# Optimization experiments

Measured on AMD Instinct MI355X. Metric: run time of the kernel, lower is better.

The kernel has to match this reference:

```python
import jax, jax.numpy as jnp
import numpy as np

N_E = 1024
E_DIM = 256
BETA = 0.25


def setup_inputs() -> dict:
    key = jax.random.key(0)
    k1, k2 = jax.random.split(key)
    z = jax.random.normal(k1, (16, E_DIM, 64, 64), dtype=jnp.float32)
    # nn.Embedding weight init: uniform(-1/n_e, 1/n_e)
    embedding = jax.random.uniform(
        k2, (N_E, E_DIM), dtype=jnp.float32, minval=-1.0 / N_E, maxval=1.0 / N_E
    )
    return {"z": z, "embedding": embedding}


def reference(z, embedding):
    n_e, e_dim = embedding.shape
    # 'b c ... -> b ... c'
    zt = jnp.moveaxis(z, 1, -1)  # [B, H, W, C]
    zf = zt.reshape(-1, e_dim)   # [N, C]
    # squared distances ||zf||^2 + ||e||^2 - 2 zf e^T  -> [N, n_e]
    d = (
        jnp.sum(zf * zf, axis=1, keepdims=True)
        + jnp.sum(embedding * embedding, axis=1)
        - 2.0 * (zf @ embedding.T)
    )
    idx = jnp.argmin(d, axis=1)  # [N] int32
    # direct embedding gather (equivalent to one-hot @ embedding)
    z_q = embedding[idx].reshape(zt.shape)  # [B, H, W, C]
    # commitment / codebook loss (reduction='mean')
    loss = jnp.mean((jax.lax.stop_gradient(z_q) - zt) ** 2) + BETA * jnp.mean(
        (z_q - jax.lax.stop_gradient(zt)) ** 2
    )
    # straight-through estimator
    z_q_st = zt + jax.lax.stop_gradient(z_q - zt)
    # perplexity from code usage histogram (equals mean of one-hot rows)
    counts = jnp.zeros((n_e,), dtype=jnp.float32).at[idx].add(1.0)
    e_mean = counts / zf.shape[0]
    perplexity = jnp.exp(-jnp.sum(e_mean * jnp.log(e_mean + 1e-10)))
    # 'b ... c -> b c ...'
    z_q_out = jnp.moveaxis(z_q_st, -1, 1)  # [B, C, H, W]
    return z_q_out, loss, perplexity, idx
```

## Files before the change

kernel.cpp:

```cpp
#include <hip/hip_runtime.h>

typedef _Float16 half8 __attribute__((ext_vector_type(8)));
typedef float f32x16 __attribute__((ext_vector_type(16)));

#define EDIM 256
#define NE   1024
#define HW   4096

#define ZQ_OFF   0
#define LOSS_OFF 16777216
#define PERP_OFF 16777217
#define IDX_OFF  16777218

#define WS_ESPH    0
#define WS_BNORM   (1024*1024)
#define WS_COUNTS  (WS_BNORM + 4096)
#define WS_COUNTER (WS_COUNTS + 4096)
#define WS_LOSS    (WS_COUNTER + 16)
#define WS_AN      (WS_LOSS + 16)
#define WS_IDX     (WS_AN + 65536*4)
#define WS_LIST    (WS_IDX + 65536*4)
#define WS_ET      (WS_LIST + 65536*4)

#define EPS 3.0e-4f
#define GEPS (512.0f * EPS)

__device__ __forceinline__ float np_half128(const float* __restrict__ p, long stride) {
#pragma clang fp contract(off)
    float r[8];
#pragma unroll
    for (int j = 0; j < 8; ++j) { float v = p[(long)j * stride]; r[j] = v * v; }
    for (int i = 8; i < 128; i += 8) {
#pragma unroll
        for (int j = 0; j < 8; ++j) { float v = p[(long)(i + j) * stride]; r[j] += v * v; }
    }
    return ((r[0] + r[1]) + (r[2] + r[3])) + ((r[4] + r[5]) + (r[6] + r[7]));
}

__global__ void k_prep_e(const float* __restrict__ e, _Float16* __restrict__ eh) {
    int t = blockIdx.x * 256 + threadIdx.x;
    int j = t >> 8, c = t & 255;
    float v = e[t] * 1024.0f;
    _Float16 h = (_Float16)v;
    int jt = j >> 7, nt = (j >> 5) & 3, lm = j & 31;
    int kc = c >> 5, r = c & 31, kh = r >> 4, hb = (r >> 3) & 1, kk = r & 7;
    int chunk = (((jt * 8 + kc) * 4 + nt) * 2 + kh) * 64 + hb * 32 + lm;
    eh[chunk * 8 + kk] = h;
}

__global__ void k_transpose(const float* __restrict__ e, float* __restrict__ eT) {
    __shared__ float tile[32][257];
    int b = blockIdx.x;
    int t = threadIdx.x;
#pragma unroll
    for (int i = 0; i < 32; ++i)
        tile[i][t] = e[(size_t)(32 * b + i) * 256 + t];
    __syncthreads();
    int jl = t & 31, cg = t >> 5;
#pragma unroll
    for (int k = 0; k < 32; ++k) {
        int c = cg * 32 + k;
        eT[(size_t)c * 1024 + 32 * b + jl] = tile[jl][c];
    }
}

__global__ void k_bnorm(const float* __restrict__ e, float* __restrict__ Bn) {
    int j = blockIdx.x * 256 + threadIdx.x;
    const float* p = e + (size_t)j * EDIM;
    Bn[j] = np_half128(p, 1) + np_half128(p + 128, 1);
}

__global__ void k_rownorm(const float* __restrict__ z, float* __restrict__ An,
                          double* __restrict__ loss_sum) {
    __shared__ double ls[4];
    int t = threadIdx.x;
    int n = blockIdx.x * 256 + t;
    int b = n >> 12, hw = n & 4095;
    const float* p = z + (size_t)b * (EDIM * HW) + hw;
    float a = np_half128(p, HW) + np_half128(p + (size_t)128 * HW, HW);
    An[n] = a;
    double s = (double)a;
#pragma unroll
    for (int sh = 1; sh < 64; sh <<= 1) s += __shfl_xor(s, sh, 64);
    if ((t & 63) == 0) ls[t >> 6] = s;
    __syncthreads();
    if (t == 0) atomicAdd(loss_sum, (ls[0] + ls[1]) + (ls[2] + ls[3]));
}

__global__ __launch_bounds__(512, 2) void k_dist(
    const float* __restrict__ z, const _Float16* __restrict__ eh,
    const float* __restrict__ Bn, int* __restrict__ idxw,
    float* __restrict__ out, int* __restrict__ counter, int* __restrict__ list,
    double* __restrict__ loss_sum, int* __restrict__ counts)
{
    __shared__ uint4  sB[2][4096];
    __shared__ double lsum[16];
    __shared__ int    lflag[256];
    __shared__ int    lcnt;
    __shared__ int    lbase;

    const int t  = threadIdx.x;
    const int w  = t >> 6;
    const int L  = t & 63;
    const int l5 = L & 31;
    const int hb = L >> 5;
    const int n0 = blockIdx.x * 256;
    const int b  = n0 >> 12, hw0 = n0 & 4095;
    const float* zb = z + (size_t)b * (EDIM * HW) + hw0;
    const int rbase = w * 32;

    if (t == 0) lcnt = 0;

    const uint4* gB4 = (const uint4*)eh;
    const int wb = t & 448;

#pragma unroll
    for (int i = 0; i < 8; ++i)
        __builtin_amdgcn_global_load_lds(
            (const __attribute__((address_space(1))) void*)(gB4 + (0 * 4096 + i * 512 + t)),
            (__attribute__((address_space(3))) void*)(&sB[0][i * 512 + wb]),
            16, 0, 0);

    half8 Ah[16];
    {
        int m = rbase + l5;
#pragma unroll
        for (int ks = 0; ks < 16; ++ks) {
            float av[8];
#pragma unroll
            for (int j = 0; j < 8; ++j)
                av[j] = zb[(ks * 16 + hb * 8 + j) * HW + m];
#pragma unroll
            for (int j = 0; j < 8; ++j)
                Ah[ks][j] = (_Float16)av[j];
        }
    }

    f32x16 acc[4];
#pragma unroll
    for (int nt = 0; nt < 4; ++nt)
#pragma unroll
        for (int r = 0; r < 16; ++r) acc[nt][r] = 0.f;

    float g1[16], g2[16]; int i1[16];
#pragma unroll
    for (int r = 0; r < 16; ++r) { g1[r] = -1e30f; g2[r] = -1e30f; i1[r] = 0; }

    __syncthreads();

    for (int jt = 0; jt < 8; ++jt) {
        const int buf = jt & 1;
        if (jt < 7) {
#pragma unroll
            for (int i = 0; i < 8; ++i)
                __builtin_amdgcn_global_load_lds(
                    (const __attribute__((address_space(1))) void*)(gB4 + ((jt + 1) * 4096 + i * 512 + t)),
                    (__attribute__((address_space(3))) void*)(&sB[buf ^ 1][i * 512 + wb]),
                    16, 0, 0);
        }

#pragma unroll
        for (int kc = 0; kc < 8; ++kc) {
#pragma unroll
            for (int kh = 0; kh < 2; ++kh) {
#pragma unroll
                for (int nt = 0; nt < 4; ++nt) {
                    half8 bh = *(const half8*)&sB[buf][((kc * 4 + nt) * 2 + kh) * 64 + L];
                    acc[nt] = __builtin_amdgcn_mfma_f32_32x32x16_f16(
                        Ah[kc * 2 + kh], bh, acc[nt], 0, 0, 0);
                }
            }
        }

        float en512[4];
#pragma unroll
        for (int nt = 0; nt < 4; ++nt)
            en512[nt] = 512.0f * Bn[jt * 128 + nt * 32 + l5];
#pragma unroll
        for (int nt = 0; nt < 4; ++nt) {
            int jc = jt * 128 + nt * 32 + l5;
#pragma unroll
            for (int r = 0; r < 16; ++r) {
                float v = acc[nt][r] - en512[nt];
                g2[r] = fmaxf(g2[r], fminf(v, g1[r]));
                bool gt = v > g1[r];
                g1[r] = fmaxf(v, g1[r]);
                i1[r] = gt ? jc : i1[r];
                acc[nt][r] = 0.f;
            }
        }

        __syncthreads();
    }

    double lossP = 0.0;
#pragma unroll
    for (int r = 0; r < 16; ++r) {
        float v1 = g1[r], v2 = g2[r]; int ii = i1[r];
#pragma unroll
        for (int s = 1; s < 32; s <<= 1) {
            float o1 = __shfl_xor(v1, s, 64);
            int   oi = __shfl_xor(ii, s, 64);
            float o2 = __shfl_xor(v2, s, 64);
            float lo = fminf(v1, o1);
            if (o1 > v1 || (o1 == v1 && oi < ii)) { v1 = o1; ii = oi; }
            v2 = fmaxf(fmaxf(v2, o2), lo);
        }
        if (l5 == 0) {
            int rloc = rbase + 4 * hb + (r & 3) + 8 * (r >> 2);
            int n = n0 + rloc;
            idxw[n] = ii;
            out[IDX_OFF + n] = (float)ii;
            atomicAdd(&counts[ii], 1);
            lossP += -(double)v1 * (1.0 / 512.0);
            if (v1 - v2 < GEPS) {
                int p = atomicAdd(&lcnt, 1);
                if (p < 256) lflag[p] = n;
            }
        }
    }
    if (l5 == 0) lsum[w * 2 + hb] = lossP;
    __syncthreads();
    if (t == 0) {
        double s = 0.0;
#pragma unroll
        for (int i = 0; i < 16; ++i) s += lsum[i];
        atomicAdd(loss_sum, s);
        lbase = lcnt ? atomicAdd(counter, lcnt) : 0;
    }
    __syncthreads();
    for (int i = t; i < lcnt; i += 512) {
        int p = lbase + i;
        if (p < 65536) list[p] = lflag[i];
    }
}

__global__ __launch_bounds__(256, 2) void k_refine(
    const float* __restrict__ z, const float* __restrict__ eT,
    const float* __restrict__ Bn, const float* __restrict__ An,
    const int* __restrict__ counter, const int* __restrict__ list,
    int* __restrict__ idxw, float* __restrict__ out,
    int* __restrict__ counts)
{
    __shared__ float zs[8][256];
    __shared__ int   ns[8];
    __shared__ float ans[8];
    __shared__ float pv[4][8];
    __shared__ int   pi[4][8];
    int t = threadIdx.x;
    int cnt = min(*counter, 65536);
    for (int li0 = blockIdx.x * 8; li0 < cnt; li0 += gridDim.x * 8) {
        int nrows = min(8, cnt - li0);
        __syncthreads();
        if (t < 8) {
            int n = (t < nrows) ? list[li0 + t] : list[li0];
            ns[t] = n; ans[t] = An[n];
        }
        __syncthreads();
#pragma unroll
        for (int u = 0; u < 8; ++u) {
            int n = ns[u];
            zs[u][t] = z[(size_t)(n >> 12) * (EDIM * HW) + (n & 4095) + t * HW];
        }
        __syncthreads();

        float D[4][8];
#pragma unroll
        for (int q = 0; q < 4; ++q)
#pragma unroll
            for (int r = 0; r < 8; ++r) D[q][r] = 0.f;

        for (int c4 = 0; c4 < 64; ++c4) {
            float4 ec[4];
#pragma unroll
            for (int cc = 0; cc < 4; ++cc)
                ec[cc] = *(const float4*)&eT[(size_t)(c4 * 4 + cc) * 1024 + 4 * t];
            float4 zr[8];
#pragma unroll
            for (int r = 0; r < 8; ++r)
                zr[r] = *(const float4*)&zs[r][c4 * 4];
#pragma unroll
            for (int cc = 0; cc < 4; ++cc) {
                const float* ep = (const float*)&ec[cc];
#pragma unroll
                for (int r = 0; r < 8; ++r) {
                    float zv = ((const float*)&zr[r])[cc];
                    D[0][r] = __builtin_fmaf(ep[0], zv, D[0][r]);
                    D[1][r] = __builtin_fmaf(ep[1], zv, D[1][r]);
                    D[2][r] = __builtin_fmaf(ep[2], zv, D[2][r]);
                    D[3][r] = __builtin_fmaf(ep[3], zv, D[3][r]);
                }
            }
        }

        float bm[8]; int bi[8];
#pragma unroll
        for (int r = 0; r < 8; ++r) { bm[r] = 1e30f; bi[r] = 1 << 30; }
        float4 bn4 = *(const float4*)&Bn[4 * t];
        {
#pragma clang fp contract(off)
#pragma unroll
            for (int q = 0; q < 4; ++q) {
                float bnj = ((const float*)&bn4)[q];
                int j = 4 * t + q;
#pragma unroll
                for (int r = 0; r < 8; ++r) {
                    float t2 = D[q][r] + D[q][r];
                    float s  = ans[r] + bnj;
                    float d  = s - t2;
                    if (d < bm[r]) { bm[r] = d; bi[r] = j; }
                }
            }
        }
        int wv = t >> 6, L = t & 63;
#pragma unroll
        for (int r = 0; r < 8; ++r) {
            float v = bm[r]; int ii = bi[r];
#pragma unroll
            for (int s = 1; s < 64; s <<= 1) {
                float ov = __shfl_xor(v, s, 64);
                int   oi = __shfl_xor(ii, s, 64);
                if (ov < v || (ov == v && oi < ii)) { v = ov; ii = oi; }
            }
            if (L == 0) { pv[wv][r] = v; pi[wv][r] = ii; }
        }
        __syncthreads();
        if (t < nrows) {
            float v = pv[0][t]; int ii = pi[0][t];
#pragma unroll
            for (int w2 = 1; w2 < 4; ++w2)
                if (pv[w2][t] < v || (pv[w2][t] == v && pi[w2][t] < ii)) { v = pv[w2][t]; ii = pi[w2][t]; }
            int n = ns[t];
            int old = idxw[n];
            if (old != ii) {
                idxw[n] = ii;
                out[IDX_OFF + n] = (float)ii;
                atomicSub(&counts[old], 1);
                atomicAdd(&counts[ii], 1);
            }
        }
    }
}

__global__ void k_gather(const float* __restrict__ e, const int* __restrict__ idxw,
                         float* __restrict__ out) {
    __shared__ int   jrow[256];
    __shared__ float Ls[8][260];
    int t = threadIdx.x;
    int rg = blockIdx.x >> 1, ch = blockIdx.x & 1;
    int n0 = rg * 256;
    int b = n0 >> 12, hw0 = n0 & 4095;
    jrow[t] = idxw[n0 + t];
    float* zqb = out + ZQ_OFF + (size_t)b * (EDIM * HW) + hw0 + (size_t)ch * 128 * HW;
    int w = t >> 6, L = t & 63;
    __syncthreads();

    for (int cc = 0; cc < 16; ++cc) {
        const float4* ep = (const float4*)(e + (size_t)jrow[t] * EDIM + ch * 128 + cc * 8);
        float4 v0 = ep[0], v1 = ep[1];
        Ls[0][t] = v0.x; Ls[1][t] = v0.y; Ls[2][t] = v0.z; Ls[3][t] = v0.w;
        Ls[4][t] = v1.x; Ls[5][t] = v1.y; Ls[6][t] = v1.z; Ls[7][t] = v1.w;
        __syncthreads();
#pragma unroll
        for (int i = 0; i < 2; ++i) {
            int c = w * 2 + i;
            float4 vv = *(const float4*)&Ls[c][L * 4];
            *(float4*)(zqb + (size_t)(cc * 8 + c) * HW + L * 4) = vv;
        }
        __syncthreads();
    }
}

__global__ void k_final(const int* __restrict__ counts, const double* __restrict__ loss_sum,
                        float* __restrict__ out) {
    __shared__ float sred[4];
    int t = threadIdx.x;
    float s = 0.f;
    for (int qq = 0; qq < 4; ++qq) {
        float p = (float)counts[qq * 256 + t] * (1.0f / 65536.0f);
        s += p * logf(p + 1e-10f);
    }
#pragma unroll
    for (int sh = 1; sh < 64; sh <<= 1) s += __shfl_xor(s, sh, 64);
    if ((t & 63) == 0) sred[t >> 6] = s;
    __syncthreads();
    if (t == 0) {
        out[PERP_OFF] = expf(-(sred[0] + sred[1] + sred[2] + sred[3]));
        out[LOSS_OFF] = (float)(*loss_sum * 1.25 / 16777216.0);
    }
}

extern "C" void kernel_launch(void* const* d_in, const int* in_sizes, int n_in,
                              void* d_out, int out_size, void* d_ws, size_t ws_size,
                              hipStream_t stream) {
    const float* z = (const float*)d_in[0];
    const float* e = (const float*)d_in[1];
    float* out = (float*)d_out;
    char* ws = (char*)d_ws;

    _Float16* eh      = (_Float16*)(ws + WS_ESPH);
    float*    Bn      = (float*)(ws + WS_BNORM);
    int*      counts  = (int*)(ws + WS_COUNTS);
    int*      counter = (int*)(ws + WS_COUNTER);
    double*   loss_sum= (double*)(ws + WS_LOSS);
    float*    An      = (float*)(ws + WS_AN);
    int*      idxw    = (int*)(ws + WS_IDX);
    int*      list    = (int*)(ws + WS_LIST);
    float*    eT      = (float*)(ws + WS_ET);

    hipMemsetAsync(ws + WS_COUNTS, 0, 4096 + 16 + 16, stream);

    k_prep_e   <<<1024, 256, 0, stream>>>(e, eh);
    k_transpose<<<32,   256, 0, stream>>>(e, eT);
    k_bnorm    <<<4,    256, 0, stream>>>(e, Bn);
    k_rownorm  <<<256,  256, 0, stream>>>(z, An, loss_sum);
    k_dist     <<<256,  512, 0, stream>>>(z, eh, Bn, idxw, out, counter, list, loss_sum, counts);
    k_refine   <<<2048, 256, 0, stream>>>(z, eT, Bn, An, counter, list, idxw, out, counts);
    k_gather   <<<512,  256, 0, stream>>>(e, idxw, out);
    k_final    <<<1,    256, 0, stream>>>(counts, loss_sum, out);
}
```

Measured before the change: 263.6 us.

## Deepen codebook LDS pipeline to four half-tile stages with explicit vmcnt waits

Splits each 128-code codebook tile into two K-halves and streams them through a four-slot LDS ring buffer, issuing each load three stages ahead. It replaces __syncthreads with manual s_waitcnt vmcnt plus s_barrier so that load latency overlaps MFMA work more deeply. It also stages the codebook norms into shared memory once, instead of reading them from global memory in every tile. The hand-written waitcnt counts must match the number of loads still outstanding, and the extra staging adds a little LDS use.

```diff
diff --git a/kernel.cpp b/kernel.cpp
--- a/kernel.cpp
+++ b/kernel.cpp
@@ -24,6 +24,9 @@
 
 #define EPS 3.0e-4f
 #define GEPS (512.0f * EPS)
+
+#define AS1 __attribute__((address_space(1)))
+#define AS3 __attribute__((address_space(3)))
 
 __device__ __forceinline__ float np_half128(const float* __restrict__ p, long stride) {
 #pragma clang fp contract(off)
@@ -87,13 +90,58 @@
     if (t == 0) atomicAdd(loss_sum, (ls[0] + ls[1]) + (ls[2] + ls[3]));
 }
 
+#define WAITV(n) asm volatile("s_waitcnt vmcnt(" #n ") lgkmcnt(0)" ::: "memory")
+#define FENCE()  asm volatile("" ::: "memory")
+#define BARRIER() __builtin_amdgcn_s_barrier()
+
+#define STAGE(S) do {                                                          \
+    _Pragma("unroll")                                                          \
+    for (int i_ = 0; i_ < 4; ++i_)                                             \
+        __builtin_amdgcn_global_load_lds(                                      \
+            (const AS1 void*)(gB4 + ((S) * 2048 + i_ * 512 + t)),              \
+            (AS3 void*)(&sB[(S) & 3][i_ * 512 + wb]), 16, 0, 0);               \
+} while (0)
+
+#define CHALF(BUF, H) do {                                                     \
+    _Pragma("unroll")                                                          \
+    for (int kcl = 0; kcl < 4; ++kcl) {                                        \
+        _Pragma("unroll")                                                      \
+        for (int kh = 0; kh < 2; ++kh) {                                       \
+            _Pragma("unroll")                                                  \
+            for (int nt = 0; nt < 4; ++nt) {                                   \
+                half8 bh = *(const half8*)&sB[BUF][((kcl * 4 + nt) * 2 + kh) * 64 + L]; \
+                acc[nt] = __builtin_amdgcn_mfma_f32_32x32x16_f16(              \
+                    Ah[(H) * 8 + kcl * 2 + kh], bh, acc[nt], 0, 0, 0);         \
+            }                                                                  \
+        }                                                                      \
+    }                                                                          \
+} while (0)
+
+#define FOLD(JT) do {                                                          \
+    _Pragma("unroll")                                                          \
+    for (int nt = 0; nt < 4; ++nt) {                                           \
+        float en = 512.0f * bnS[(JT) * 128 + nt * 32 + l5];                    \
+        int jc = (JT) * 128 + nt * 32 + l5;                                    \
+        _Pragma("unroll")                                                      \
+        for (int r = 0; r < 16; ++r) {                                         \
+            float v = acc[nt][r] - en;                                         \
+            g2[r] = fmaxf(g2[r], fminf(v, g1[r]));                             \
+            bool gt = v > g1[r];                                               \
+            g1[r] = fmaxf(v, g1[r]);                                           \
+            i1[r] = gt ? jc : i1[r];                                           \
+            acc[nt][r] = 0.f;                                                  \
+        }                                                                      \
+    }                                                                          \
+} while (0)
+
 __global__ __launch_bounds__(512, 2) void k_dist(
     const float* __restrict__ z, const _Float16* __restrict__ eh,
     const float* __restrict__ Bn, int* __restrict__ idxw,
     float* __restrict__ out, int* __restrict__ counter, int* __restrict__ list,
     double* __restrict__ loss_sum, int* __restrict__ counts)
 {
-    __shared__ uint4  sB[2][4096];
+    __shared__ uint4  sB[4][2048];
+    __shared__ float  bnS[1024];
     __shared__ double lsum[16];
     __shared__ int    lflag[256];
     __shared__ int    lcnt;
@@ -110,16 +158,13 @@
     const int rbase = w * 32;
 
     if (t == 0) lcnt = 0;
+    bnS[t]       = Bn[t];
+    bnS[t + 512] = Bn[t + 512];
 
     const uint4* gB4 = (const uint4*)eh;
     const int wb = t & 448;
 
-#pragma unroll
-    for (int i = 0; i < 8; ++i)
-        __builtin_amdgcn_global_load_lds(
-            (const __attribute__((address_space(1))) void*)(gB4 + (0 * 4096 + i * 512 + t)),
-            (__attribute__((address_space(3))) void*)(&sB[0][i * 512 + wb]),
-            16, 0, 0);
+    STAGE(0); STAGE(1); STAGE(2);
 
     half8 Ah[16];
     {
@@ -146,52 +191,26 @@
 #pragma unroll
     for (int r = 0; r < 16; ++r) { g1[r] = -1e30f; g2[r] = -1e30f; i1[r] = 0; }
 
-    __syncthreads();
-
-    for (int jt = 0; jt < 8; ++jt) {
-        const int buf = jt & 1;
-        if (jt < 7) {
-#pragma unroll
-            for (int i = 0; i < 8; ++i)
-                __builtin_amdgcn_global_load_lds(
-                    (const __attribute__((address_space(1))) void*)(gB4 + ((jt + 1) * 4096 + i * 512 + t)),
-                    (__attribute__((address_space(3))) void*)(&sB[buf ^ 1][i * 512 + wb]),
-                    16, 0, 0);
-        }
-
-#pragma unroll
-        for (int kc = 0; kc < 8; ++kc) {
-#pragma unroll
-            for (int kh = 0; kh < 2; ++kh) {
-#pragma unroll
-                for (int nt = 0; nt < 4; ++nt) {
-                    half8 bh = *(const half8*)&sB[buf][((kc * 4 + nt) * 2 + kh) * 64 + L];
-                    acc[nt] = __builtin_amdgcn_mfma_f32_32x32x16_f16(
-                        Ah[kc * 2 + kh], bh, acc[nt], 0, 0, 0);
-                }
-            }
-        }
-
-        float en512[4];
-#pragma unroll
-        for (int nt = 0; nt < 4; ++nt)
-            en512[nt] = 512.0f * Bn[jt * 128 + nt * 32 + l5];
-#pragma unroll
-        for (int nt = 0; nt < 4; ++nt) {
-            int jc = jt * 128 + nt * 32 + l5;
-#pragma unroll
-            for (int r = 0; r < 16; ++r) {
-                float v = acc[nt][r] - en512[nt];
-                g2[r] = fmaxf(g2[r], fminf(v, g1[r]));
-                bool gt = v > g1[r];
-                g1[r] = fmaxf(v, g1[r]);
-                i1[r] = gt ? jc : i1[r];
-                acc[nt][r] = 0.f;
-            }
-        }
-
-        __syncthreads();
-    }
+    for (int jt = 0; jt < 6; ++jt) {
+        WAITV(8); BARRIER(); FENCE();
+        STAGE(2 * jt + 3);
+        CHALF((2 * jt) & 3, 0);
+        WAITV(8); BARRIER(); FENCE();
+        STAGE(2 * jt + 4);
+        CHALF((2 * jt + 1) & 3, 1);
+        FOLD(jt);
+    }
+    WAITV(8); BARRIER(); FENCE();
+    STAGE(15);
+    CHALF(0, 0);
+    WAITV(8); BARRIER(); FENCE();
+    CHALF(1, 1);
+    FOLD(6);
+    WAITV(4); BARRIER(); FENCE();
+    CHALF(2, 0);
+    WAITV(0); BARRIER(); FENCE();
+    CHALF(3, 1);
+    FOLD(7);
 
     double lossP = 0.0;
 #pragma unroll
```

Result: no change. 262.5 us (-0.4%).
